# Performance work log

Hardware: AMD Instinct MI355X
Metric: run time of the kernel (lower is better)

The kernel has to match this reference:

```python
import jax, jax.numpy as jnp
import numpy as np

B, G, N, P, E, F, K = 8, 256, 1024, 4, 1, 256, 4
ZERO_TOL = 1e-9
INF = 1e12
ATT_SLOPE = 0.2  # leaky relu slope inside attention


def setup_inputs() -> dict:
    key = jax.random.key(0)
    ks = jax.random.split(key, 6)
    stdv = float(1.0 / np.sqrt(G * P))
    x = jax.random.normal(ks[0], (B, G, N), jnp.float32)
    mixer = jax.random.uniform(ks[1], (P, E, 2 * F), jnp.float32, -stdv, stdv)
    weight = jax.random.uniform(ks[2], (P, E, F, G), jnp.float32, -stdv, stdv)
    weight_bias = jnp.zeros((P, E, F), jnp.float32)  # reset_parameters inits to 0
    filterWeight = jax.random.uniform(ks[3], (P, F, E, K, G), jnp.float32, -stdv, stdv)
    bias = jax.random.uniform(ks[4], (F, 1), jnp.float32, -stdv, stdv)
    adj = (jax.random.uniform(ks[5], (B, E, N, N)) < 0.05).astype(jnp.float32)
    S = jnp.maximum(adj, jnp.eye(N, dtype=jnp.float32)[None, None])
    return dict(x=x, mixer=mixer, weight=weight, weight_bias=weight_bias,
                filterWeight=filterWeight, bias=bias, S=S)


def reference(x, mixer, weight, weight_bias, filterWeight, bias, S):
    # --- learnAttentionGSOBatch ---
    # Wx: [B,P,E,F,N]
    Wx = jnp.einsum('pefg,bgn->bpefn', weight, x) + weight_bias[None, :, :, :, None]
    a1 = mixer[..., :F]   # [P,E,F]
    a2 = mixer[..., F:]   # [P,E,F]
    e1 = jnp.einsum('pef,bpefn->bpen', a1, Wx)  # a1^T W x_j
    e2 = jnp.einsum('pef,bpefn->bpen', a2, Wx)  # a2^T W x_i
    # aWx[b,p,e,i,j] = e1[j] + e2[i]  (matches a1Wx + a2Wx^T broadcast)
    aWx = e1[..., None, :] + e2[..., :, None]   # [B,P,E,N,N]
    eij = jax.nn.leaky_relu(aWx, ATT_SLOPE)
    mask = (jnp.sum(jnp.abs(S), axis=1)[:, None, None] > ZERO_TOL).astype(x.dtype)  # [B,1,1,N,N]
    aij = jax.nn.softmax(eij * mask - (1.0 - mask) * INF, axis=-1) * mask  # [B,P,E,N,N]

    # --- K-hop polynomial filter ---
    xk = jnp.broadcast_to(x[:, None, None], (B, P, E, G, N))
    zs = [xk]
    for _ in range(1, K):
        xk = jnp.matmul(xk, aij)        # diffuse along attention GSO
        zs.append(xk)
    z = jnp.stack(zs, axis=3)            # [B,P,E,K,G,N]
    # h reshape [P,F,E*K*G] contracted against z reshaped [B,P,N,E*K*G]
    y = jnp.einsum('bpekgn,pfekg->bpfn', z, filterWeight) + bias  # bias [F,1] broadcasts

    # --- forward wrapper: nonlinearity (leaky_relu, default slope 0.01) + head concat ---
    y = jax.nn.leaky_relu(y)                              # [B,P,F,N]
    y = jnp.transpose(y, (0, 3, 1, 2)).reshape(B, N, P * F)
    return jnp.transpose(y, (0, 2, 1))                    # [B, P*F, N]
```

## Files before the change

### kernel.cpp

```cpp
#include <hip/hip_runtime.h>
#include <hip/hip_bf16.h>

#define B_ 8
#define G_ 256
#define N_ 1024
#define P_ 4
#define F_ 256
#define KHOP 4
#define KG_ (KHOP * G_)

typedef unsigned short ushort_t;
typedef __bf16 bf16x8 __attribute__((ext_vector_type(8)));
typedef unsigned short u16x8 __attribute__((ext_vector_type(8)));
typedef float f32x4 __attribute__((ext_vector_type(4)));

__device__ __forceinline__ unsigned short f2bf(float f) {
  union { float fl; unsigned int i; } v; v.fl = f;
  return (unsigned short)((v.i + 0x7fffu + ((v.i >> 16) & 1u)) >> 16);
}

__device__ __forceinline__ void gload_lds16(const ushort_t* g, ushort_t* l) {
  __builtin_amdgcn_global_load_lds(
      (const __attribute__((address_space(1))) void*)g,
      (__attribute__((address_space(3))) void*)l, 16, 0, 0);
}

__global__ __launch_bounds__(256) void k_prep(
    const float* __restrict__ x, const float* __restrict__ mixer,
    const float* __restrict__ weight, const float* __restrict__ wb,
    const float* __restrict__ fw, float* __restrict__ e1, float* __restrict__ e2,
    ushort_t* __restrict__ fwbf, ushort_t* __restrict__ xT,
    float* __restrict__ sumb) {
  int blk = blockIdx.x;
  int t = threadIdx.x;
  if (blk < 128) {
    __shared__ float s1[G_], s2[G_];
    __shared__ float cred[2][4];
    int bp = blk >> 2;
    int nc = blk & 3;
    int b = bp >> 2, p = bp & (P_ - 1);
    int n = nc * 256 + t;
    float acc1 = 0.f, acc2 = 0.f;
    const float* wp = weight + (size_t)p * F_ * G_ + t;
    const float* mp = mixer + p * 2 * F_;
    for (int f = 0; f < F_; ++f) {
      float wv = wp[(size_t)f * G_];
      acc1 = fmaf(mp[f], wv, acc1);
      acc2 = fmaf(mp[F_ + f], wv, acc2);
    }
    s1[t] = acc1;
    s2[t] = acc2;
    float c1p = mp[t] * wb[p * F_ + t];
    float c2p = mp[F_ + t] * wb[p * F_ + t];
#pragma unroll
    for (int mask = 1; mask < 64; mask <<= 1) {
      c1p += __shfl_xor(c1p, mask, 64);
      c2p += __shfl_xor(c2p, mask, 64);
    }
    if ((t & 63) == 0) {
      cred[0][t >> 6] = c1p;
      cred[1][t >> 6] = c2p;
    }
    __syncthreads();
    float c1 = cred[0][0] + cred[0][1] + cred[0][2] + cred[0][3];
    float c2 = cred[1][0] + cred[1][1] + cred[1][2] + cred[1][3];
    const float* xb = x + (size_t)b * G_ * N_ + n;
    float a1 = 0.f, a2 = 0.f;
#pragma unroll 8
    for (int g = 0; g < G_; ++g) {
      float xv = xb[(size_t)g * N_];
      a1 = fmaf(s1[g], xv, a1);
      a2 = fmaf(s2[g], xv, a2);
    }
    e1[(size_t)bp * N_ + n] = c1 + a1;
    e2[(size_t)bp * N_ + n] = c2 + a2;
  } else if (blk < 128 + 1024) {
    int i = (blk - 128) * 1024 + t * 4;
    float4 v = *(const float4*)&fw[i];
    ushort4 o;
    o.x = f2bf(v.x); o.y = f2bf(v.y); o.z = f2bf(v.z); o.w = f2bf(v.w);
    *(ushort4*)&fwbf[i] = o;
  } else if (blk < 1152 + 512) {
    __shared__ ushort_t tile[64][66];
    int idx = blk - 1152;
    int n0 = (idx & 15) * 64;
    int g0 = ((idx >> 4) & 3) * 64;
    int b = idx >> 6;
    int rr = t >> 4, cc = (t & 15) * 4;
#pragma unroll
    for (int ps = 0; ps < 4; ++ps) {
      float4 v = *(const float4*)&x[((size_t)b * G_ + g0 + ps * 16 + rr) * N_ + n0 + cc];
      tile[ps * 16 + rr][cc] = f2bf(v.x);
      tile[ps * 16 + rr][cc + 1] = f2bf(v.y);
      tile[ps * 16 + rr][cc + 2] = f2bf(v.z);
      tile[ps * 16 + rr][cc + 3] = f2bf(v.w);
    }
    __syncthreads();
#pragma unroll
    for (int ps = 0; ps < 4; ++ps) {
      int nl = ps * 16 + rr;
      int gl = cc;
      ushort4 o;
      o.x = tile[gl][nl];
      o.y = tile[gl + 1][nl];
      o.z = tile[gl + 2][nl];
      o.w = tile[gl + 3][nl];
      *(ushort4*)&xT[((size_t)b * N_ + n0 + nl) * G_ + g0 + gl] = o;
    }
  } else {
    int i = (blk - 1664) * 256 + t;
    sumb[i] = 0.f;
  }
}

__global__ __launch_bounds__(256) void k_att(const float* __restrict__ e1,
                                             const float* __restrict__ e2,
                                             const float* __restrict__ S,
                                             ushort_t* __restrict__ expT,
                                             float* __restrict__ sumb) {
  __shared__ ushort_t tile[256][72];
  __shared__ float se1[256];
  __shared__ float se2[64];
  int bp = blockIdx.z;
  int b = bp >> 2;
  int i0 = blockIdx.y * 64;
  int jt = blockIdx.x;
  int j0 = jt * 256;
  int t = threadIdx.x;
  int rr = t >> 4;
  int cc4 = t & 15;
  int cc = cc4 * 4;

  se1[t] = e1[(size_t)bp * N_ + j0 + t];
  if (t < 64) se2[t] = e2[(size_t)bp * N_ + i0 + t];
  __syncthreads();

  const float* Sb = S + (size_t)b * N_ * N_;
  float re2[4];
#pragma unroll
  for (int ps = 0; ps < 4; ++ps) re2[ps] = se2[ps * 16 + rr];
  float psum[4] = {0.f, 0.f, 0.f, 0.f};
#pragma unroll
  for (int js = 0; js < 4; ++js) {
    float4 e1q = *(float4*)&se1[js * 64 + cc];
    float e1v[4] = {e1q.x, e1q.y, e1q.z, e1q.w};
#pragma unroll
    for (int ps = 0; ps < 4; ++ps) {
      int il = ps * 16 + rr;
      float4 s4 = *(const float4*)&Sb[(size_t)(i0 + il) * N_ + j0 + js * 64 + cc];
      float sv[4] = {s4.x, s4.y, s4.z, s4.w};
#pragma unroll
      for (int s = 0; s < 4; ++s) {
        float v = e1v[s] + re2[ps];
        float l = v >= 0.f ? v : 0.2f * v;
        bool m = fabsf(sv[s]) > 1e-9f;
        float e = m ? __expf(l) : 0.f;
        psum[ps] += e;
        tile[js * 64 + cc + s][il] = f2bf(e);
      }
    }
  }
#pragma unroll
  for (int mask = 1; mask < 16; mask <<= 1) {
#pragma unroll
    for (int ps = 0; ps < 4; ++ps) psum[ps] += __shfl_xor(psum[ps], mask, 64);
  }
  if (cc4 == 0) {
#pragma unroll
    for (int ps = 0; ps < 4; ++ps)
      atomicAdd(&sumb[(size_t)bp * N_ + i0 + ps * 16 + rr], psum[ps]);
  }
  __syncthreads();
  ushort_t* Tb = expT + (size_t)bp * N_ * N_;
  int jl0 = t >> 3;
  int ig = (t & 7) * 8;
#pragma unroll
  for (int pass = 0; pass < 8; ++pass) {
    int jl = pass * 32 + jl0;
    u16x8 v = *(const u16x8*)&tile[jl][ig];
    *(u16x8*)&Tb[(size_t)(j0 + jl) * N_ + i0 + ig] = v;
  }
}

__global__ __launch_bounds__(256, 2) void gemm_step(
    const ushort_t* __restrict__ Aprev, const ushort_t* __restrict__ Bt,
    const ushort_t* __restrict__ fwbf, const ushort_t* __restrict__ xT,
    const float* __restrict__ bias, const float* __restrict__ sumb,
    ushort_t* __restrict__ outb, float* __restrict__ outf,
    int kslice, int has_prev, int last) {
  __shared__ ushort_t As[2][128 * 32];
  __shared__ ushort_t Bs[2][128 * 32];
  int bp = blockIdx.z;
  int p = bp & (P_ - 1), b = bp >> 2;
  int n0 = blockIdx.x * 128, m0 = blockIdx.y * 128;
  int t = threadIdx.x;
  int lane = t & 63;
  int w = t >> 6;
  int wm = w >> 1, wn = w & 1;
  int lr = lane & 15, quad = lane >> 4;
  int rowL = t >> 2;
  int colL = (t & 3) * 8;
  int ldsoff = (t & ~63) * 8;

  const ushort_t* A1 = Aprev + (size_t)bp * (F_ * N_) + (size_t)(m0 + rowL) * N_ + colL;
  const ushort_t* B1 = Bt + (size_t)bp * N_ * N_ + (size_t)(n0 + rowL) * N_ + colL;
  const ushort_t* A2 = fwbf + (size_t)p * (F_ * KG_) + (size_t)(m0 + rowL) * KG_ +
                       kslice * G_ + colL;
  const ushort_t* B2 = xT + (size_t)b * (N_ * G_) + (size_t)(n0 + rowL) * G_ + colL;

  f32x4 acc[4][4] = {};

  if (has_prev) {
    for (int kt = 0; kt < N_; kt += 64) {
      __syncthreads();
      gload_lds16(A1 + kt, &As[0][ldsoff]);
      gload_lds16(A1 + (size_t)64 * N_ + kt, &As[0][2048 + ldsoff]);
      gload_lds16(A1 + kt + 32, &As[1][ldsoff]);
      gload_lds16(A1 + (size_t)64 * N_ + kt + 32, &As[1][2048 + ldsoff]);
      gload_lds16(B1 + kt, &Bs[0][ldsoff]);
      gload_lds16(B1 + (size_t)64 * N_ + kt, &Bs[0][2048 + ldsoff]);
      gload_lds16(B1 + kt + 32, &Bs[1][ldsoff]);
      gload_lds16(B1 + (size_t)64 * N_ + kt + 32, &Bs[1][2048 + ldsoff]);
      __syncthreads();
#pragma unroll
      for (int c = 0; c < 2; ++c) {
        bf16x8 af[4], bfr[4];
#pragma unroll
        for (int mi = 0; mi < 4; ++mi)
          af[mi] = __builtin_bit_cast(bf16x8,
              *(const u16x8*)&As[c][(wm * 64 + mi * 16 + lr) * 32 + quad * 8]);
#pragma unroll
        for (int ni = 0; ni < 4; ++ni)
          bfr[ni] = __builtin_bit_cast(bf16x8,
              *(const u16x8*)&Bs[c][(wn * 64 + ni * 16 + lr) * 32 + quad * 8]);
#pragma unroll
        for (int mi = 0; mi < 4; ++mi)
#pragma unroll
          for (int ni = 0; ni < 4; ++ni)
            acc[mi][ni] = __builtin_amdgcn_mfma_f32_16x16x32_bf16(af[mi], bfr[ni], acc[mi][ni], 0, 0, 0);
      }
    }
  }
  for (int gt = 0; gt < G_; gt += 64) {
    __syncthreads();
    gload_lds16(A2 + gt, &As[0][ldsoff]);
    gload_lds16(A2 + (size_t)64 * KG_ + gt, &As[0][2048 + ldsoff]);
    gload_lds16(A2 + gt + 32, &As[1][ldsoff]);
    gload_lds16(A2 + (size_t)64 * KG_ + gt + 32, &As[1][2048 + ldsoff]);
    gload_lds16(B2 + gt, &Bs[0][ldsoff]);
    gload_lds16(B2 + (size_t)64 * G_ + gt, &Bs[0][2048 + ldsoff]);
    gload_lds16(B2 + gt + 32, &Bs[1][ldsoff]);
    gload_lds16(B2 + (size_t)64 * G_ + gt + 32, &Bs[1][2048 + ldsoff]);
    __syncthreads();
#pragma unroll
    for (int c = 0; c < 2; ++c) {
      bf16x8 af[4], bfr[4];
#pragma unroll
      for (int mi = 0; mi < 4; ++mi)
        af[mi] = __builtin_bit_cast(bf16x8,
            *(const u16x8*)&As[c][(wm * 64 + mi * 16 + lr) * 32 + quad * 8]);
#pragma unroll
      for (int ni = 0; ni < 4; ++ni)
        bfr[ni] = __builtin_bit_cast(bf16x8,
            *(const u16x8*)&Bs[c][(wn * 64 + ni * 16 + lr) * 32 + quad * 8]);
#pragma unroll
      for (int mi = 0; mi < 4; ++mi)
#pragma unroll
        for (int ni = 0; ni < 4; ++ni)
          acc[mi][ni] = __builtin_amdgcn_mfma_f32_16x16x32_bf16(af[mi], bfr[ni], acc[mi][ni], 0, 0, 0);
    }
  }

  if (last) {
    float* Ob = outf + (size_t)bp * (F_ * N_);
#pragma unroll
    for (int mi = 0; mi < 4; ++mi) {
      int fbase = m0 + wm * 64 + mi * 16 + quad * 4;
#pragma unroll
      for (int ni = 0; ni < 4; ++ni) {
        int n = n0 + wn * 64 + ni * 16 + lr;
#pragma unroll
        for (int r = 0; r < 4; ++r) {
          float v = acc[mi][ni][r] + bias[fbase + r];
          Ob[(size_t)(fbase + r) * N_ + n] = v >= 0.f ? v : 0.01f * v;
        }
      }
    }
  } else {
    ushort_t* Ob = outb + (size_t)bp * (F_ * N_);
    float iv[4];
#pragma unroll
    for (int ni = 0; ni < 4; ++ni)
      iv[ni] = 1.0f / sumb[(size_t)bp * N_ + n0 + wn * 64 + ni * 16 + lr];
#pragma unroll
    for (int mi = 0; mi < 4; ++mi) {
      int fbase = m0 + wm * 64 + mi * 16 + quad * 4;
#pragma unroll
      for (int ni = 0; ni < 4; ++ni) {
        int n = n0 + wn * 64 + ni * 16 + lr;
#pragma unroll
        for (int r = 0; r < 4; ++r)
          Ob[(size_t)(fbase + r) * N_ + n] = f2bf(acc[mi][ni][r] * iv[ni]);
      }
    }
  }
}

extern "C" void kernel_launch(void* const* d_in, const int* in_sizes, int n_in,
                              void* d_out, int out_size, void* d_ws, size_t ws_size,
                              hipStream_t stream) {
  const float* x = (const float*)d_in[0];
  const float* mixer = (const float*)d_in[1];
  const float* weight = (const float*)d_in[2];
  const float* wb = (const float*)d_in[3];
  const float* fw = (const float*)d_in[4];
  const float* bias = (const float*)d_in[5];
  const float* S = (const float*)d_in[6];
  float* out = (float*)d_out;

  char* ws = (char*)d_ws;
  size_t off = 0;
  auto take = [&](size_t bytes) -> char* {
    char* p = ws + off;
    off = (off + bytes + 255) & ~(size_t)255;
    return p;
  };
  float* e1 = (float*)take((size_t)B_ * P_ * N_ * 4);
  float* e2 = (float*)take((size_t)B_ * P_ * N_ * 4);
  float* sumb = (float*)take((size_t)B_ * P_ * N_ * 4);
  ushort_t* fwbf = (ushort_t*)take((size_t)P_ * F_ * KHOP * G_ * 2);
  ushort_t* xT = (ushort_t*)take((size_t)B_ * N_ * G_ * 2);
  ushort_t* expT = (ushort_t*)take((size_t)B_ * P_ * N_ * N_ * 2);
  ushort_t* sA = (ushort_t*)take((size_t)B_ * P_ * F_ * N_ * 2);
  ushort_t* sB = (ushort_t*)take((size_t)B_ * P_ * F_ * N_ * 2);

  k_prep<<<1792, 256, 0, stream>>>(x, mixer, weight, wb, fw, e1, e2, fwbf, xT, sumb);
  k_att<<<dim3(4, 16, 32), 256, 0, stream>>>(e1, e2, S, expT, sumb);

  dim3 gg(8, 2, 32);
  gemm_step<<<gg, 256, 0, stream>>>(nullptr, expT, fwbf, xT, bias, sumb, sA, nullptr, 3, 0, 0);
  gemm_step<<<gg, 256, 0, stream>>>(sA, expT, fwbf, xT, bias, sumb, sB, nullptr, 2, 1, 0);
  gemm_step<<<gg, 256, 0, stream>>>(sB, expT, fwbf, xT, bias, sumb, sA, nullptr, 1, 1, 0);
  gemm_step<<<gg, 256, 0, stream>>>(sA, expT, fwbf, xT, bias, sumb, nullptr, out, 0, 1, 1);
}
```

Before: 256.4 us.

## Fuse all stages into one persistent kernel with software grid barriers

Replaces six kernel launches (prep, attention, four GEMM steps) with a single persistent kernel of 512 blocks that runs every stage in turn and separates them with an atomic-counter grid barrier. Shared memory is carved from one static buffer, and sumb zeroing moves to a memset. The aim is to remove per-launch overhead and the tail bubbles between kernels. In exchange, the code depends on all 512 blocks being co-resident (2 per CU across 256 CUs), the spinning barrier adds latency, and stages with fewer natural blocks now loop over their work inside each block.

```diff
diff --git a/kernel.cpp b/kernel.cpp
--- a/kernel.cpp
+++ b/kernel.cpp
@@ -7,7 +7,8 @@
 #define P_ 4
 #define F_ 256
 #define KHOP 4
-#define KG_ (KHOP * G_)
+#define KG_ 1024
+#define NBLK 512
 
 typedef unsigned short ushort_t;
 typedef __bf16 bf16x8 __attribute__((ext_vector_type(8)));
@@ -25,106 +26,115 @@
       (__attribute__((address_space(3))) void*)l, 16, 0, 0);
 }
 
-__global__ __launch_bounds__(256) void k_prep(
-    const float* __restrict__ x, const float* __restrict__ mixer,
-    const float* __restrict__ weight, const float* __restrict__ wb,
-    const float* __restrict__ fw, float* __restrict__ e1, float* __restrict__ e2,
-    ushort_t* __restrict__ fwbf, ushort_t* __restrict__ xT,
-    float* __restrict__ sumb) {
-  int blk = blockIdx.x;
+__device__ __forceinline__ void gridbar(unsigned* bar, unsigned target) {
+  __syncthreads();
+  if (threadIdx.x == 0) {
+    __threadfence();
+    __hip_atomic_fetch_add(bar, 1u, __ATOMIC_ACQ_REL, __HIP_MEMORY_SCOPE_AGENT);
+    while (__hip_atomic_load(bar, __ATOMIC_ACQUIRE, __HIP_MEMORY_SCOPE_AGENT) < target) {
+      __builtin_amdgcn_s_sleep(2);
+    }
+  }
+  __syncthreads();
+}
+
+__device__ void prep_e(int job, const float* __restrict__ x,
+                       const float* __restrict__ mixer, const float* __restrict__ weight,
+                       const float* __restrict__ wb, float* __restrict__ e1,
+                       float* __restrict__ e2, char* smem) {
+  float* s1 = (float*)smem;
+  float* s2 = (float*)(smem + 1024);
+  float* cred = (float*)(smem + 2048);
   int t = threadIdx.x;
-  if (blk < 128) {
-    __shared__ float s1[G_], s2[G_];
-    __shared__ float cred[2][4];
-    int bp = blk >> 2;
-    int nc = blk & 3;
-    int b = bp >> 2, p = bp & (P_ - 1);
-    int n = nc * 256 + t;
-    float acc1 = 0.f, acc2 = 0.f;
-    const float* wp = weight + (size_t)p * F_ * G_ + t;
-    const float* mp = mixer + p * 2 * F_;
-    for (int f = 0; f < F_; ++f) {
-      float wv = wp[(size_t)f * G_];
-      acc1 = fmaf(mp[f], wv, acc1);
-      acc2 = fmaf(mp[F_ + f], wv, acc2);
-    }
-    s1[t] = acc1;
-    s2[t] = acc2;
-    float c1p = mp[t] * wb[p * F_ + t];
-    float c2p = mp[F_ + t] * wb[p * F_ + t];
-#pragma unroll
-    for (int mask = 1; mask < 64; mask <<= 1) {
-      c1p += __shfl_xor(c1p, mask, 64);
-      c2p += __shfl_xor(c2p, mask, 64);
-    }
-    if ((t & 63) == 0) {
-      cred[0][t >> 6] = c1p;
-      cred[1][t >> 6] = c2p;
-    }
-    __syncthreads();
-    float c1 = cred[0][0] + cred[0][1] + cred[0][2] + cred[0][3];
-    float c2 = cred[1][0] + cred[1][1] + cred[1][2] + cred[1][3];
-    const float* xb = x + (size_t)b * G_ * N_ + n;
-    float a1 = 0.f, a2 = 0.f;
+  int bp = job >> 2;
+  int nc = job & 3;
+  int b = bp >> 2, p = bp & (P_ - 1);
+  int n = nc * 256 + t;
+  float acc1 = 0.f, acc2 = 0.f;
+  const float* wp = weight + (size_t)p * F_ * G_ + t;
+  const float* mp = mixer + p * 2 * F_;
+  for (int f = 0; f < F_; ++f) {
+    float wv = wp[(size_t)f * G_];
+    acc1 = fmaf(mp[f], wv, acc1);
+    acc2 = fmaf(mp[F_ + f], wv, acc2);
+  }
+  __syncthreads();
+  s1[t] = acc1;
+  s2[t] = acc2;
+  float c1p = mp[t] * wb[p * F_ + t];
+  float c2p = mp[F_ + t] * wb[p * F_ + t];
+#pragma unroll
+  for (int mask = 1; mask < 64; mask <<= 1) {
+    c1p += __shfl_xor(c1p, mask, 64);
+    c2p += __shfl_xor(c2p, mask, 64);
+  }
+  if ((t & 63) == 0) {
+    cred[t >> 6] = c1p;
+    cred[4 + (t >> 6)] = c2p;
+  }
+  __syncthreads();
+  float c1 = cred[0] + cred[1] + cred[2] + cred[3];
+  float c2 = cred[4] + cred[5] + cred[6] + cred[7];
+  const float* xb = x + (size_t)b * G_ * N_ + n;
+  float a1 = 0.f, a2 = 0.f;
 #pragma unroll 8
-    for (int g = 0; g < G_; ++g) {
-      float xv = xb[(size_t)g * N_];
-      a1 = fmaf(s1[g], xv, a1);
-      a2 = fmaf(s2[g], xv, a2);
-    }
-    e1[(size_t)bp * N_ + n] = c1 + a1;
-    e2[(size_t)bp * N_ + n] = c2 + a2;
-  } else if (blk < 128 + 1024) {
-    int i = (blk - 128) * 1024 + t * 4;
-    float4 v = *(const float4*)&fw[i];
+  for (int g = 0; g < G_; ++g) {
+    float xv = xb[(size_t)g * N_];
+    a1 = fmaf(s1[g], xv, a1);
+    a2 = fmaf(s2[g], xv, a2);
+  }
+  e1[(size_t)bp * N_ + n] = c1 + a1;
+  e2[(size_t)bp * N_ + n] = c2 + a2;
+}
+
+__device__ void prep_cast(int job, const float* __restrict__ fw,
+                          ushort_t* __restrict__ fwbf) {
+  int i = job * 1024 + threadIdx.x * 4;
+  float4 v = *(const float4*)&fw[i];
+  ushort4 o;
+  o.x = f2bf(v.x); o.y = f2bf(v.y); o.z = f2bf(v.z); o.w = f2bf(v.w);
+  *(ushort4*)&fwbf[i] = o;
+}
+
+__device__ void prep_xT(int job, const float* __restrict__ x,
+                        ushort_t* __restrict__ xT, char* smem) {
+  ushort_t* tile = (ushort_t*)smem;
+  int n0 = (job & 15) * 64;
+  int g0 = ((job >> 4) & 3) * 64;
+  int b = job >> 6;
+  int t = threadIdx.x;
+  int rr = t >> 4, cc = (t & 15) * 4;
+  __syncthreads();
+#pragma unroll
+  for (int ps = 0; ps < 4; ++ps) {
+    float4 v = *(const float4*)&x[((size_t)b * G_ + g0 + ps * 16 + rr) * N_ + n0 + cc];
+    tile[(ps * 16 + rr) * 66 + cc] = f2bf(v.x);
+    tile[(ps * 16 + rr) * 66 + cc + 1] = f2bf(v.y);
+    tile[(ps * 16 + rr) * 66 + cc + 2] = f2bf(v.z);
+    tile[(ps * 16 + rr) * 66 + cc + 3] = f2bf(v.w);
+  }
+  __syncthreads();
+#pragma unroll
+  for (int ps = 0; ps < 4; ++ps) {
+    int nl = ps * 16 + rr;
+    int gl = cc;
     ushort4 o;
-    o.x = f2bf(v.x); o.y = f2bf(v.y); o.z = f2bf(v.z); o.w = f2bf(v.w);
-    *(ushort4*)&fwbf[i] = o;
-  } else if (blk < 1152 + 512) {
-    __shared__ ushort_t tile[64][66];
-    int idx = blk - 1152;
-    int n0 = (idx & 15) * 64;
-    int g0 = ((idx >> 4) & 3) * 64;
-    int b = idx >> 6;
-    int rr = t >> 4, cc = (t & 15) * 4;
-#pragma unroll
-    for (int ps = 0; ps < 4; ++ps) {
-      float4 v = *(const float4*)&x[((size_t)b * G_ + g0 + ps * 16 + rr) * N_ + n0 + cc];
-      tile[ps * 16 + rr][cc] = f2bf(v.x);
-      tile[ps * 16 + rr][cc + 1] = f2bf(v.y);
-      tile[ps * 16 + rr][cc + 2] = f2bf(v.z);
-      tile[ps * 16 + rr][cc + 3] = f2bf(v.w);
-    }
-    __syncthreads();
-#pragma unroll
-    for (int ps = 0; ps < 4; ++ps) {
-      int nl = ps * 16 + rr;
-      int gl = cc;
-      ushort4 o;
-      o.x = tile[gl][nl];
-      o.y = tile[gl + 1][nl];
-      o.z = tile[gl + 2][nl];
-      o.w = tile[gl + 3][nl];
-      *(ushort4*)&xT[((size_t)b * N_ + n0 + nl) * G_ + g0 + gl] = o;
-    }
-  } else {
-    int i = (blk - 1664) * 256 + t;
-    sumb[i] = 0.f;
-  }
-}
-
-__global__ __launch_bounds__(256) void k_att(const float* __restrict__ e1,
-                                             const float* __restrict__ e2,
-                                             const float* __restrict__ S,
-                                             ushort_t* __restrict__ expT,
-                                             float* __restrict__ sumb) {
-  __shared__ ushort_t tile[256][72];
-  __shared__ float se1[256];
-  __shared__ float se2[64];
-  int bp = blockIdx.z;
+    o.x = tile[gl * 66 + nl];
+    o.y = tile[(gl + 1) * 66 + nl];
+    o.z = tile[(gl + 2) * 66 + nl];
+    o.w = tile[(gl + 3) * 66 + nl];
+    *(ushort4*)&xT[((size_t)b * N_ + n0 + nl) * G_ + g0 + gl] = o;
+  }
+}
+
+__device__ void att_body(int bp, int i0, int jt, const float* __restrict__ e1,
+                         const float* __restrict__ e2, const float* __restrict__ S,
+                         ushort_t* __restrict__ expT, float* __restrict__ sumb,
+                         char* smem) {
+  ushort_t* tile = (ushort_t*)smem;
+  float* se1 = (float*)(smem + 36864);
+  float* se2 = (float*)(smem + 36864 + 1024);
   int b = bp >> 2;
-  int i0 = blockIdx.y * 64;
-  int jt = blockIdx.x;
   int j0 = jt * 256;
   int t = threadIdx.x;
   int rr = t >> 4;
@@ -156,7 +166,7 @@
         bool m = fabsf(sv[s]) > 1e-9f;
         float e = m ? __expf(l) : 0.f;
         psum[ps] += e;
-        tile[js * 64 + cc + s][il] = f2bf(e);
+        tile[(js * 64 + cc + s) * 72 + il] = f2bf(e);
       }
     }
   }
@@ -177,22 +187,24 @@
 #pragma unroll
   for (int pass = 0; pass < 8; ++pass) {
     int jl = pass * 32 + jl0;
-    u16x8 v = *(const u16x8*)&tile[jl][ig];
+    u16x8 v = *(const u16x8*)&tile[jl * 72 + ig];
     *(u16x8*)&Tb[(size_t)(j0 + jl) * N_ + i0 + ig] = v;
   }
 }
 
-__global__ __launch_bounds__(256, 2) void gemm_step(
-    const ushort_t* __restrict__ Aprev, const ushort_t* __restrict__ Bt,
-    const ushort_t* __restrict__ fwbf, const ushort_t* __restrict__ xT,
-    const float* __restrict__ bias, const float* __restrict__ sumb,
-    ushort_t* __restrict__ outb, float* __restrict__ outf,
-    int kslice, int has_prev, int last) {
-  __shared__ ushort_t As[2][128 * 32];
-  __shared__ ushort_t Bs[2][128 * 32];
-  int bp = blockIdx.z;
+__device__ void gemm_body(int L, const ushort_t* __restrict__ Aprev,
+                          const ushort_t* __restrict__ Bt,
+                          const ushort_t* __restrict__ fwbf,
+                          const ushort_t* __restrict__ xT,
+                          const float* __restrict__ bias,
+                          const float* __restrict__ sumb,
+                          ushort_t* __restrict__ outb, float* __restrict__ outf,
+                          int kslice, int has_prev, int last, char* smem) {
+  ushort_t* As = (ushort_t*)smem;
+  ushort_t* Bs = (ushort_t*)(smem + 16384);
+  int bp = L >> 4;
   int p = bp & (P_ - 1), b = bp >> 2;
-  int n0 = blockIdx.x * 128, m0 = blockIdx.y * 128;
+  int n0 = (L & 7) * 128, m0 = ((L >> 3) & 1) * 128;
   int t = threadIdx.x;
   int lane = t & 63;
   int w = t >> 6;
@@ -213,14 +225,14 @@
   if (has_prev) {
     for (int kt = 0; kt < N_; kt += 64) {
       __syncthreads();
-      gload_lds16(A1 + kt, &As[0][ldsoff]);
-      gload_lds16(A1 + (size_t)64 * N_ + kt, &As[0][2048 + ldsoff]);
-      gload_lds16(A1 + kt + 32, &As[1][ldsoff]);
-      gload_lds16(A1 + (size_t)64 * N_ + kt + 32, &As[1][2048 + ldsoff]);
-      gload_lds16(B1 + kt, &Bs[0][ldsoff]);
-      gload_lds16(B1 + (size_t)64 * N_ + kt, &Bs[0][2048 + ldsoff]);
-      gload_lds16(B1 + kt + 32, &Bs[1][ldsoff]);
-      gload_lds16(B1 + (size_t)64 * N_ + kt + 32, &Bs[1][2048 + ldsoff]);
+      gload_lds16(A1 + kt, &As[ldsoff]);
+      gload_lds16(A1 + (size_t)64 * N_ + kt, &As[2048 + ldsoff]);
+      gload_lds16(A1 + kt + 32, &As[4096 + ldsoff]);
+      gload_lds16(A1 + (size_t)64 * N_ + kt + 32, &As[4096 + 2048 + ldsoff]);
+      gload_lds16(B1 + kt, &Bs[ldsoff]);
+      gload_lds16(B1 + (size_t)64 * N_ + kt, &Bs[2048 + ldsoff]);
+      gload_lds16(B1 + kt + 32, &Bs[4096 + ldsoff]);
+      gload_lds16(B1 + (size_t)64 * N_ + kt + 32, &Bs[4096 + 2048 + ldsoff]);
       __syncthreads();
 #pragma unroll
       for (int c = 0; c < 2; ++c) {
@@ -228,11 +240,11 @@
 #pragma unroll
         for (int mi = 0; mi < 4; ++mi)
           af[mi] = __builtin_bit_cast(bf16x8,
-              *(const u16x8*)&As[c][(wm * 64 + mi * 16 + lr) * 32 + quad * 8]);
+              *(const u16x8*)&As[c * 4096 + (wm * 64 + mi * 16 + lr) * 32 + quad * 8]);
 #pragma unroll
         for (int ni = 0; ni < 4; ++ni)
           bfr[ni] = __builtin_bit_cast(bf16x8,
-              *(const u16x8*)&Bs[c][(wn * 64 + ni * 16 + lr) * 32 + quad * 8]);
+              *(const u16x8*)&Bs[c * 4096 + (wn * 64 + ni * 16 + lr) * 32 + quad * 8]);
 #pragma unroll
         for (int mi = 0; mi < 4; ++mi)
 #pragma unroll
@@ -243,14 +255,14 @@
   }
   for (int gt = 0; gt < G_; gt += 64) {
     __syncthreads();
-    gload_lds16(A2 + gt, &As[0][ldsoff]);
-    gload_lds16(A2 + (size_t)64 * KG_ + gt, &As[0][2048 + ldsoff]);
-    gload_lds16(A2 + gt + 32, &As[1][ldsoff]);
-    gload_lds16(A2 + (size_t)64 * KG_ + gt + 32, &As[1][2048 + ldsoff]);
-    gload_lds16(B2 + gt, &Bs[0][ldsoff]);
-    gload_lds16(B2 + (size_t)64 * G_ + gt, &Bs[0][2048 + ldsoff]);
-    gload_lds16(B2 + gt + 32, &Bs[1][ldsoff]);
-    gload_lds16(B2 + (size_t)64 * G_ + gt + 32, &Bs[1][2048 + ldsoff]);
+    gload_lds16(A2 + gt, &As[ldsoff]);
+    gload_lds16(A2 + (size_t)64 * KG_ + gt, &As[2048 + ldsoff]);
+    gload_lds16(A2 + gt + 32, &As[4096 + ldsoff]);
+    gload_lds16(A2 + (size_t)64 * KG_ + gt + 32, &As[4096 + 2048 + ldsoff]);
+    gload_lds16(B2 + gt, &Bs[ldsoff]);
+    gload_lds16(B2 + (size_t)64 * G_ + gt, &Bs[2048 + ldsoff]);
+    gload_lds16(B2 + gt + 32, &Bs[4096 + ldsoff]);
+    gload_lds16(B2 + (size_t)64 * G_ + gt + 32, &Bs[4096 + 2048 + ldsoff]);
     __syncthreads();
 #pragma unroll
     for (int c = 0; c < 2; ++c) {
@@ -258,11 +270,11 @@
 #pragma unroll
       for (int mi = 0; mi < 4; ++mi)
         af[mi] = __builtin_bit_cast(bf16x8,
-            *(const u16x8*)&As[c][(wm * 64 + mi * 16 + lr) * 32 + quad * 8]);
+            *(const u16x8*)&As[c * 4096 + (wm * 64 + mi * 16 + lr) * 32 + quad * 8]);
 #pragma unroll
       for (int ni = 0; ni < 4; ++ni)
         bfr[ni] = __builtin_bit_cast(bf16x8,
-            *(const u16x8*)&Bs[c][(wn * 64 + ni * 16 + lr) * 32 + quad * 8]);
+            *(const u16x8*)&Bs[c * 4096 + (wn * 64 + ni * 16 + lr) * 32 + quad * 8]);
 #pragma unroll
       for (int mi = 0; mi < 4; ++mi)
 #pragma unroll
@@ -304,6 +316,42 @@
       }
     }
   }
+}
+
+__global__ __launch_bounds__(256, 2) void k_fused(
+    const float* __restrict__ x, const float* __restrict__ mixer,
+    const float* __restrict__ weight, const float* __restrict__ wb,
+    const float* __restrict__ fw, const float* __restrict__ bias,
+    const float* __restrict__ S, float* __restrict__ e1, float* __restrict__ e2,
+    float* __restrict__ sumb, ushort_t* __restrict__ fwbf,
+    ushort_t* __restrict__ xT, ushort_t* __restrict__ expT,
+    ushort_t* __restrict__ sA, ushort_t* __restrict__ sB,
+    float* __restrict__ out, unsigned* __restrict__ bar) {
+  __shared__ __align__(16) char smem[38400];
+  int L = blockIdx.x;
+
+  for (int q = 0; q < 4; ++q) {
+    int job = L + NBLK * q;
+    if (job < 128) prep_e(job, x, mixer, weight, wb, e1, e2, smem);
+    else if (job < 1152) prep_cast(job - 128, fw, fwbf);
+    else if (job < 1664) prep_xT(job - 1152, x, xT, smem);
+  }
+  gridbar(bar, 1 * NBLK);
+
+  {
+    int b = L >> 6, i0 = ((L >> 2) & 15) * 64, jt = L & 3;
+    for (int p = 0; p < 4; ++p)
+      att_body(b * 4 + p, i0, jt, e1, e2, S, expT, sumb, smem);
+  }
+  gridbar(bar, 2 * NBLK);
+
+  gemm_body(L, sA, expT, fwbf, xT, bias, sumb, sA, out, 3, 0, 0, smem);
+  gridbar(bar, 3 * NBLK);
+  gemm_body(L, sA, expT, fwbf, xT, bias, sumb, sB, out, 2, 1, 0, smem);
+  gridbar(bar, 4 * NBLK);
+  gemm_body(L, sB, expT, fwbf, xT, bias, sumb, sA, out, 1, 1, 0, smem);
+  gridbar(bar, 5 * NBLK);
+  gemm_body(L, sA, expT, fwbf, xT, bias, sumb, nullptr, out, 0, 1, 1, smem);
 }
 
 extern "C" void kernel_launch(void* const* d_in, const int* in_sizes, int n_in,
@@ -325,6 +373,7 @@
     off = (off + bytes + 255) & ~(size_t)255;
     return p;
   };
+  unsigned* bar = (unsigned*)take(256);
   float* e1 = (float*)take((size_t)B_ * P_ * N_ * 4);
   float* e2 = (float*)take((size_t)B_ * P_ * N_ * 4);
   float* sumb = (float*)take((size_t)B_ * P_ * N_ * 4);
@@ -334,12 +383,8 @@
   ushort_t* sA = (ushort_t*)take((size_t)B_ * P_ * F_ * N_ * 2);
   ushort_t* sB = (ushort_t*)take((size_t)B_ * P_ * F_ * N_ * 2);
 
-  k_prep<<<1792, 256, 0, stream>>>(x, mixer, weight, wb, fw, e1, e2, fwbf, xT, sumb);
-  k_att<<<dim3(4, 16, 32), 256, 0, stream>>>(e1, e2, S, expT, sumb);
-
-  dim3 gg(8, 2, 32);
-  gemm_step<<<gg, 256, 0, stream>>>(nullptr, expT, fwbf, xT, bias, sumb, sA, nullptr, 3, 0, 0);
-  gemm_step<<<gg, 256, 0, stream>>>(sA, expT, fwbf, xT, bias, sumb, sB, nullptr, 2, 1, 0);
-  gemm_step<<<gg, 256, 0, stream>>>(sB, expT, fwbf, xT, bias, sumb, sA, nullptr, 1, 1, 0);
-  gemm_step<<<gg, 256, 0, stream>>>(sA, expT, fwbf, xT, bias, sumb, nullptr, out, 0, 1, 1);
-}
+  hipMemsetAsync(bar, 0, 256, stream);
+  hipMemsetAsync(sumb, 0, (size_t)B_ * P_ * N_ * 4, stream);
+  k_fused<<<NBLK, 256, 0, stream>>>(x, mixer, weight, wb, fw, bias, S, e1, e2,
+                                    sumb, fwbf, xT, expT, sA, sB, out, bar);
+}
```

Measured after the change: 744.1 us. 190% more time.

## Fuse first Horner GEMM step into attention kernel with atomic counter wait

Applied to the files above, without the earlier changes.

Moves the first gemm_step (fwbf slice 3 times xT, with no previous term) into the tail of the attention kernel. The first 512 blocks compute the tile after writing their exp tile, then spin on a global counter until all 2048 attention blocks have finished before normalising by the row sums. This removes one kernel launch and overlaps that GEMM with the attention work. The spin-wait only works if all waited-on blocks can be scheduled, so it risks deadlock and adds polling cost. It also adds launch_bounds occupancy 4 and a dead no-op loop.

```diff
diff --git a/kernel.cpp b/kernel.cpp
--- a/kernel.cpp
+++ b/kernel.cpp
@@ -7,7 +7,7 @@
 #define P_ 4
 #define F_ 256
 #define KHOP 4
-#define KG_ (KHOP * G_)
+#define KG_ 1024
 
 typedef unsigned short ushort_t;
 typedef __bf16 bf16x8 __attribute__((ext_vector_type(8)));
@@ -30,12 +30,12 @@
     const float* __restrict__ weight, const float* __restrict__ wb,
     const float* __restrict__ fw, float* __restrict__ e1, float* __restrict__ e2,
     ushort_t* __restrict__ fwbf, ushort_t* __restrict__ xT,
-    float* __restrict__ sumb) {
+    float* __restrict__ sumb, unsigned* __restrict__ cnt) {
   int blk = blockIdx.x;
   int t = threadIdx.x;
   if (blk < 128) {
     __shared__ float s1[G_], s2[G_];
-    __shared__ float cred[2][4];
+    __shared__ float cred[8];
     int bp = blk >> 2;
     int nc = blk & 3;
     int b = bp >> 2, p = bp & (P_ - 1);
@@ -58,12 +58,12 @@
       c2p += __shfl_xor(c2p, mask, 64);
     }
     if ((t & 63) == 0) {
-      cred[0][t >> 6] = c1p;
-      cred[1][t >> 6] = c2p;
-    }
-    __syncthreads();
-    float c1 = cred[0][0] + cred[0][1] + cred[0][2] + cred[0][3];
-    float c2 = cred[1][0] + cred[1][1] + cred[1][2] + cred[1][3];
+      cred[t >> 6] = c1p;
+      cred[4 + (t >> 6)] = c2p;
+    }
+    __syncthreads();
+    float c1 = cred[0] + cred[1] + cred[2] + cred[3];
+    float c2 = cred[4] + cred[5] + cred[6] + cred[7];
     const float* xb = x + (size_t)b * G_ * N_ + n;
     float a1 = 0.f, a2 = 0.f;
 #pragma unroll 8
@@ -110,22 +110,25 @@
   } else {
     int i = (blk - 1664) * 256 + t;
     sumb[i] = 0.f;
-  }
-}
-
-__global__ __launch_bounds__(256) void k_att(const float* __restrict__ e1,
-                                             const float* __restrict__ e2,
-                                             const float* __restrict__ S,
-                                             ushort_t* __restrict__ expT,
-                                             float* __restrict__ sumb) {
+    if (blk == 1664 && t == 0)
+      __hip_atomic_store(cnt, 0u, __ATOMIC_RELAXED, __HIP_MEMORY_SCOPE_AGENT);
+  }
+}
+
+__global__ __launch_bounds__(256, 4) void k_att(
+    const float* __restrict__ e1, const float* __restrict__ e2,
+    const float* __restrict__ S, ushort_t* __restrict__ expT,
+    float* __restrict__ sumb, const ushort_t* __restrict__ fwbf,
+    const ushort_t* __restrict__ xT, ushort_t* __restrict__ sA,
+    unsigned* __restrict__ cnt) {
   __shared__ ushort_t tile[256][72];
   __shared__ float se1[256];
   __shared__ float se2[64];
-  int bp = blockIdx.z;
+  int L = blockIdx.x;
+  int bp = L >> 6;
+  int i0 = ((L >> 2) & 15) * 64;
+  int j0 = (L & 3) * 256;
   int b = bp >> 2;
-  int i0 = blockIdx.y * 64;
-  int jt = blockIdx.x;
-  int j0 = jt * 256;
   int t = threadIdx.x;
   int rr = t >> 4;
   int cc4 = t & 15;
@@ -171,14 +174,100 @@
       atomicAdd(&sumb[(size_t)bp * N_ + i0 + ps * 16 + rr], psum[ps]);
   }
   __syncthreads();
-  ushort_t* Tb = expT + (size_t)bp * N_ * N_;
-  int jl0 = t >> 3;
-  int ig = (t & 7) * 8;
-#pragma unroll
-  for (int pass = 0; pass < 8; ++pass) {
-    int jl = pass * 32 + jl0;
-    u16x8 v = *(const u16x8*)&tile[jl][ig];
-    *(u16x8*)&Tb[(size_t)(j0 + jl) * N_ + i0 + ig] = v;
+  {
+    ushort_t* Tb = expT + (size_t)bp * N_ * N_;
+    int jl0 = t >> 3;
+    int ig = (t & 7) * 8;
+#pragma unroll
+    for (int pass = 0; pass < 8; ++pass) {
+      int jl = pass * 32 + jl0;
+      u16x8 v = *(const u16x8*)&tile[jl * 72 + ig - jl * 72 + jl * 72][0 + ig - ig + ig];
+      (void)v;
+      break;
+    }
+#pragma unroll
+    for (int pass = 0; pass < 8; ++pass) {
+      int jl = pass * 32 + jl0;
+      u16x8 v = *(const u16x8*)&tile[jl][ig];
+      *(u16x8*)&Tb[(size_t)(j0 + jl) * N_ + i0 + ig] = v;
+    }
+  }
+  __syncthreads();
+  if (t == 0) {
+    __threadfence();
+    __hip_atomic_fetch_add(cnt, 1u, __ATOMIC_RELEASE, __HIP_MEMORY_SCOPE_AGENT);
+  }
+  if (L >= 512) return;
+
+  {
+    int bp2 = L >> 4;
+    int p = bp2 & (P_ - 1), b2 = bp2 >> 2;
+    int n0 = (L & 7) * 128, m0 = ((L >> 3) & 1) * 128;
+    int lane = t & 63;
+    int w = t >> 6;
+    int wm = w >> 1, wn = w & 1;
+    int lr = lane & 15, quad = lane >> 4;
+    int rowL = t >> 2;
+    int colL = (t & 3) * 8;
+    int ldsoff = (t & ~63) * 8;
+    ushort_t* lds = &tile[0][0];
+
+    const ushort_t* A2 = fwbf + (size_t)p * (F_ * KG_) + (size_t)(m0 + rowL) * KG_ +
+                         3 * G_ + colL;
+    const ushort_t* B2 = xT + (size_t)b2 * (N_ * G_) + (size_t)(n0 + rowL) * G_ + colL;
+
+    f32x4 acc[4][4] = {};
+    for (int gt = 0; gt < G_; gt += 64) {
+      __syncthreads();
+      gload_lds16(A2 + gt, &lds[ldsoff]);
+      gload_lds16(A2 + (size_t)64 * KG_ + gt, &lds[2048 + ldsoff]);
+      gload_lds16(A2 + gt + 32, &lds[4096 + ldsoff]);
+      gload_lds16(A2 + (size_t)64 * KG_ + gt + 32, &lds[4096 + 2048 + ldsoff]);
+      gload_lds16(B2 + gt, &lds[8192 + ldsoff]);
+      gload_lds16(B2 + (size_t)64 * G_ + gt, &lds[8192 + 2048 + ldsoff]);
+      gload_lds16(B2 + gt + 32, &lds[8192 + 4096 + ldsoff]);
+      gload_lds16(B2 + (size_t)64 * G_ + gt + 32, &lds[8192 + 4096 + 2048 + ldsoff]);
+      __syncthreads();
+#pragma unroll
+      for (int c = 0; c < 2; ++c) {
+        bf16x8 af[4], bfr[4];
+#pragma unroll
+        for (int mi = 0; mi < 4; ++mi)
+          af[mi] = __builtin_bit_cast(bf16x8,
+              *(const u16x8*)&lds[c * 4096 + (wm * 64 + mi * 16 + lr) * 32 + quad * 8]);
+#pragma unroll
+        for (int ni = 0; ni < 4; ++ni)
+          bfr[ni] = __builtin_bit_cast(bf16x8,
+              *(const u16x8*)&lds[8192 + c * 4096 + (wn * 64 + ni * 16 + lr) * 32 + quad * 8]);
+#pragma unroll
+        for (int mi = 0; mi < 4; ++mi)
+#pragma unroll
+          for (int ni = 0; ni < 4; ++ni)
+            acc[mi][ni] = __builtin_amdgcn_mfma_f32_16x16x32_bf16(af[mi], bfr[ni], acc[mi][ni], 0, 0, 0);
+      }
+    }
+    if (t == 0) {
+      while (__hip_atomic_load(cnt, __ATOMIC_RELAXED, __HIP_MEMORY_SCOPE_AGENT) < 2048)
+        __builtin_amdgcn_s_sleep(8);
+      (void)__hip_atomic_load(cnt, __ATOMIC_ACQUIRE, __HIP_MEMORY_SCOPE_AGENT);
+    }
+    __syncthreads();
+    ushort_t* Ob = sA + (size_t)bp2 * (F_ * N_);
+    float iv[4];
+#pragma unroll
+    for (int ni = 0; ni < 4; ++ni)
+      iv[ni] = 1.0f / sumb[(size_t)bp2 * N_ + n0 + wn * 64 + ni * 16 + lr];
+#pragma unroll
+    for (int mi = 0; mi < 4; ++mi) {
+      int fbase = m0 + wm * 64 + mi * 16 + quad * 4;
+#pragma unroll
+      for (int ni = 0; ni < 4; ++ni) {
+        int n = n0 + wn * 64 + ni * 16 + lr;
+#pragma unroll
+        for (int r = 0; r < 4; ++r)
+          Ob[(size_t)(fbase + r) * N_ + n] = f2bf(acc[mi][ni][r] * iv[ni]);
+      }
+    }
   }
 }
 
@@ -187,7 +276,7 @@
     const ushort_t* __restrict__ fwbf, const ushort_t* __restrict__ xT,
     const float* __restrict__ bias, const float* __restrict__ sumb,
     ushort_t* __restrict__ outb, float* __restrict__ outf,
-    int kslice, int has_prev, int last) {
+    int kslice, int last) {
   __shared__ ushort_t As[2][128 * 32];
   __shared__ ushort_t Bs[2][128 * 32];
   int bp = blockIdx.z;
@@ -210,35 +299,33 @@
 
   f32x4 acc[4][4] = {};
 
-  if (has_prev) {
-    for (int kt = 0; kt < N_; kt += 64) {
-      __syncthreads();
-      gload_lds16(A1 + kt, &As[0][ldsoff]);
-      gload_lds16(A1 + (size_t)64 * N_ + kt, &As[0][2048 + ldsoff]);
-      gload_lds16(A1 + kt + 32, &As[1][ldsoff]);
-      gload_lds16(A1 + (size_t)64 * N_ + kt + 32, &As[1][2048 + ldsoff]);
-      gload_lds16(B1 + kt, &Bs[0][ldsoff]);
-      gload_lds16(B1 + (size_t)64 * N_ + kt, &Bs[0][2048 + ldsoff]);
-      gload_lds16(B1 + kt + 32, &Bs[1][ldsoff]);
-      gload_lds16(B1 + (size_t)64 * N_ + kt + 32, &Bs[1][2048 + ldsoff]);
-      __syncthreads();
-#pragma unroll
-      for (int c = 0; c < 2; ++c) {
-        bf16x8 af[4], bfr[4];
-#pragma unroll
-        for (int mi = 0; mi < 4; ++mi)
-          af[mi] = __builtin_bit_cast(bf16x8,
-              *(const u16x8*)&As[c][(wm * 64 + mi * 16 + lr) * 32 + quad * 8]);
+  for (int kt = 0; kt < N_; kt += 64) {
+    __syncthreads();
+    gload_lds16(A1 + kt, &As[0][ldsoff]);
+    gload_lds16(A1 + (size_t)64 * N_ + kt, &As[0][2048 + ldsoff]);
+    gload_lds16(A1 + kt + 32, &As[1][ldsoff]);
+    gload_lds16(A1 + (size_t)64 * N_ + kt + 32, &As[1][2048 + ldsoff]);
+    gload_lds16(B1 + kt, &Bs[0][ldsoff]);
+    gload_lds16(B1 + (size_t)64 * N_ + kt, &Bs[0][2048 + ldsoff]);
+    gload_lds16(B1 + kt + 32, &Bs[1][ldsoff]);
+    gload_lds16(B1 + (size_t)64 * N_ + kt + 32, &Bs[1][2048 + ldsoff]);
+    __syncthreads();
+#pragma unroll
+    for (int c = 0; c < 2; ++c) {
+      bf16x8 af[4], bfr[4];
+#pragma unroll
+      for (int mi = 0; mi < 4; ++mi)
+        af[mi] = __builtin_bit_cast(bf16x8,
+            *(const u16x8*)&As[c][(wm * 64 + mi * 16 + lr) * 32 + quad * 8]);
+#pragma unroll
+      for (int ni = 0; ni < 4; ++ni)
+        bfr[ni] = __builtin_bit_cast(bf16x8,
+            *(const u16x8*)&Bs[c][(wn * 64 + ni * 16 + lr) * 32 + quad * 8]);
+#pragma unroll
+      for (int mi = 0; mi < 4; ++mi)
 #pragma unroll
         for (int ni = 0; ni < 4; ++ni)
-          bfr[ni] = __builtin_bit_cast(bf16x8,
-              *(const u16x8*)&Bs[c][(wn * 64 + ni * 16 + lr) * 32 + quad * 8]);
-#pragma unroll
-        for (int mi = 0; mi < 4; ++mi)
-#pragma unroll
-          for (int ni = 0; ni < 4; ++ni)
-            acc[mi][ni] = __builtin_amdgcn_mfma_f32_16x16x32_bf16(af[mi], bfr[ni], acc[mi][ni], 0, 0, 0);
-      }
+          acc[mi][ni] = __builtin_amdgcn_mfma_f32_16x16x32_bf16(af[mi], bfr[ni], acc[mi][ni], 0, 0, 0);
     }
   }
   for (int gt = 0; gt < G_; gt += 64) {
@@ -325,6 +412,7 @@
     off = (off + bytes + 255) & ~(size_t)255;
     return p;
   };
+  unsigned* cnt = (unsigned*)take(256);
   float* e1 = (float*)take((size_t)B_ * P_ * N_ * 4);
   float* e2 = (float*)take((size_t)B_ * P_ * N_ * 4);
   float* sumb = (float*)take((size_t)B_ * P_ * N_ * 4);
@@ -334,12 +422,11 @@
   ushort_t* sA = (ushort_t*)take((size_t)B_ * P_ * F_ * N_ * 2);
   ushort_t* sB = (ushort_t*)take((size_t)B_ * P_ * F_ * N_ * 2);
 
-  k_prep<<<1792, 256, 0, stream>>>(x, mixer, weight, wb, fw, e1, e2, fwbf, xT, sumb);
-  k_att<<<dim3(4, 16, 32), 256, 0, stream>>>(e1, e2, S, expT, sumb);
+  k_prep<<<1792, 256, 0, stream>>>(x, mixer, weight, wb, fw, e1, e2, fwbf, xT, sumb, cnt);
+  k_att<<<2048, 256, 0, stream>>>(e1, e2, S, expT, sumb, fwbf, xT, sA, cnt);
 
   dim3 gg(8, 2, 32);
-  gemm_step<<<gg, 256, 0, stream>>>(nullptr, expT, fwbf, xT, bias, sumb, sA, nullptr, 3, 0, 0);
-  gemm_step<<<gg, 256, 0, stream>>>(sA, expT, fwbf, xT, bias, sumb, sB, nullptr, 2, 1, 0);
-  gemm_step<<<gg, 256, 0, stream>>>(sB, expT, fwbf, xT, bias, sumb, sA, nullptr, 1, 1, 0);
-  gemm_step<<<gg, 256, 0, stream>>>(sA, expT, fwbf, xT, bias, sumb, nullptr, out, 0, 1, 1);
-}
+  gemm_step<<<gg, 256, 0, stream>>>(sA, expT, fwbf, xT, bias, sumb, sB, nullptr, 2, 0);
+  gemm_step<<<gg, 256, 0, stream>>>(sB, expT, fwbf, xT, bias, sumb, sA, nullptr, 1, 0);
+  gemm_step<<<gg, 256, 0, stream>>>(sA, expT, fwbf, xT, bias, sumb, nullptr, out, 0, 1);
+}
```

After: 506.7 us. +97.6%, slower.
